# Kernel optimization log

Measured on AMD Instinct MI355X. Metric: run time of the kernel, lower is better.

## Reference

```python
import jax, jax.numpy as jnp
import numpy as np

K = 1254  # top-k patches kept by the gate


def setup_inputs() -> dict:
    key = jax.random.key(0)
    k1, k2 = jax.random.split(key)
    x = jax.random.normal(k1, (16, 224, 224, 64), dtype=jnp.float32)
    gating_kernel = jax.random.normal(k2, (2, 2, 64, 1), dtype=jnp.float32) * 0.05
    return {"x": x, "gating_kernel": gating_kernel}


def reference(x, gating_kernel):
    # x: [B, H, W, C] (NHWC), gating_kernel: [kh, kw, C, 1]
    B, H, W, C = x.shape
    kh, kw = gating_kernel.shape[0], gating_kernel.shape[1]
    # 1-channel gating conv, stride == kernel size, 'valid' padding -> [B, Ho, Wo]
    g = jax.lax.conv_general_dilated(
        x, gating_kernel,
        window_strides=(kh, kw), padding='VALID',
        dimension_numbers=('NHWC', 'HWIO', 'NHWC'))[..., 0]
    Ho, Wo = g.shape[1], g.shape[2]
    n = Ho * Wo
    flat = g.reshape(B, n)
    # top-k patch scores per image; activation is linear (None) in this config
    values, indices = jax.lax.top_k(flat, K)
    # scatter-sum values back to a dense [B, n] gate (top_k indices are distinct,
    # so add == unsorted_segment_sum exactly)
    batch_idx = jnp.arange(B)[:, None]  # [B, 1]
    gate = jnp.zeros((B, n), dtype=x.dtype).at[batch_idx, indices].add(values)
    gate = gate.reshape(B, Ho, Wo)
    # broadcast each patch score over its kh x kw spatial block and all C channels
    gate_full = jnp.broadcast_to(
        gate[:, :, None, :, None], (B, Ho, kh, Wo, kw)).reshape(B, H, W)
    return x * gate_full[..., None]
```

## Files before the change

kernel.cpp:

```cpp
#include <hip/hip_runtime.h>
#include <hip/hip_bf16.h>
#include <stdint.h>

#define BATCH   16
#define HDIM    224
#define WDIM    224
#define CDIM    64
#define HO      112
#define WO      112
#define NPATCH  (HO * WO)
#define KSEL    1254
#define ROWF    (WDIM * CDIM)
#define PERTHR  49
#define ROWF4   (WDIM * 16)
#define BLKROW  14

typedef float f32x4 __attribute__((ext_vector_type(4)));

__global__ __launch_bounds__(256) void conv_gate_kernel(
    const float* __restrict__ x, const float* __restrict__ wk,
    float* __restrict__ g) {
  const int tid = threadIdx.x;
  const int lane = tid & 31;
  const int p = blockIdx.x * 8 + (tid >> 5);

  const int b   = p / NPATCH;
  const int rem = p - b * NPATCH;
  const int ho  = rem / WO;
  const int wo  = rem - ho * WO;

  const float4 w0 = *reinterpret_cast<const float4*>(wk + lane * 4);
  const float4 w1 = *reinterpret_cast<const float4*>(wk + 128 + lane * 4);

  const long row0 = (long)(b * HDIM + 2 * ho) * ROWF + wo * 128 + lane * 4;
  const float4 a0 = *reinterpret_cast<const float4*>(x + row0);
  const float4 a1 = *reinterpret_cast<const float4*>(x + row0 + ROWF);

  float partial = a0.x * w0.x + a0.y * w0.y + a0.z * w0.z + a0.w * w0.w
                + a1.x * w1.x + a1.y * w1.y + a1.z * w1.z + a1.w * w1.w;

  #pragma unroll
  for (int off = 16; off > 0; off >>= 1)
    partial += __shfl_down(partial, off, 32);

  if (lane == 0) g[p] = partial;
}

__global__ __launch_bounds__(256) void select_kernel(
    const float* __restrict__ g, float* __restrict__ gate) {
  __shared__ int wave_cnt[4];
  __shared__ uint32_t sh_T;
  __shared__ int sh_cg;
  __shared__ int eq_list[256];
  __shared__ int eq_count;

  const int b = blockIdx.x;
  const int tid = threadIdx.x;
  const float* __restrict__ gb  = g    + b * NPATCH;
  float* __restrict__       gtb = gate + b * NPATCH;

  uint32_t key[PERTHR];
  #pragma unroll
  for (int j = 0; j < PERTHR; ++j) {
    uint32_t u = __float_as_uint(gb[tid + j * 256]);
    key[j] = (u & 0x80000000u) ? ~u : (u | 0x80000000u);
  }
  if (tid == 0) eq_count = 0;

  uint32_t T = 0;
  for (int bit = 31; bit >= 0; --bit) {
    const uint32_t cand = T | (1u << bit);
    int c = 0;
    #pragma unroll
    for (int j = 0; j < PERTHR; ++j) c += (key[j] >= cand) ? 1 : 0;
    #pragma unroll
    for (int off = 32; off > 0; off >>= 1) c += __shfl_down(c, off, 64);
    if ((tid & 63) == 0) wave_cnt[tid >> 6] = c;
    __syncthreads();
    if (tid == 0) {
      int tot = wave_cnt[0] + wave_cnt[1] + wave_cnt[2] + wave_cnt[3];
      sh_T = (tot >= KSEL) ? cand : T;
    }
    __syncthreads();
    T = sh_T;
  }

  {
    int c = 0;
    #pragma unroll
    for (int j = 0; j < PERTHR; ++j) c += (key[j] > T) ? 1 : 0;
    #pragma unroll
    for (int off = 32; off > 0; off >>= 1) c += __shfl_down(c, off, 64);
    if ((tid & 63) == 0) wave_cnt[tid >> 6] = c;
    __syncthreads();
    if (tid == 0) sh_cg = wave_cnt[0] + wave_cnt[1] + wave_cnt[2] + wave_cnt[3];
    __syncthreads();
  }
  const int krem = KSEL - sh_cg;

  #pragma unroll
  for (int j = 0; j < PERTHR; ++j) {
    const int i = tid + j * 256;
    const uint32_t k = key[j];
    float v = 0.0f;
    if (k > T) {
      uint32_t u = (k & 0x80000000u) ? (k & 0x7FFFFFFFu) : ~k;
      v = __uint_as_float(u);
    }
    gtb[i] = v;
    if (k == T) {
      int pos = atomicAdd(&eq_count, 1);
      if (pos < 256) eq_list[pos] = i;
    }
  }
  __syncthreads();

  if (tid == 0) {
    const int ec = eq_count;
    if (ec <= 256) {
      for (int i = 0; i < ec; ++i) {
        int mn = i;
        for (int j = i + 1; j < ec; ++j)
          if (eq_list[j] < eq_list[mn]) mn = j;
        int t = eq_list[mn]; eq_list[mn] = eq_list[i]; eq_list[i] = t;
      }
      for (int i = 0; i < ec && i < krem; ++i) {
        int idx = eq_list[i];
        uint32_t u = (T & 0x80000000u) ? (T & 0x7FFFFFFFu) : ~T;
        gtb[idx] = __uint_as_float(u);
      }
    } else {
      int kept = 0;
      for (int i = 0; i < NPATCH; ++i) {
        uint32_t u = __float_as_uint(gb[i]);
        uint32_t k = (u & 0x80000000u) ? ~u : (u | 0x80000000u);
        if (k == T) { gtb[i] = (kept < krem) ? gb[i] : 0.0f; ++kept; }
      }
    }
  }
}

__global__ __launch_bounds__(256) void apply_gate_kernel(
    const float* __restrict__ x, const float* __restrict__ gate,
    float* __restrict__ out) {
  const int bi = blockIdx.x;
  const int rowblk = bi % BLKROW;
  const int rowid  = bi / BLKROW;
  const int h = rowid % HDIM;
  const int b = rowid / HDIM;

  const int v4row = rowblk * 256 + threadIdx.x;
  const int w = v4row >> 4;
  const int gidx = b * NPATCH + (h >> 1) * WO + (w >> 1);

  const float gv = gate[gidx];
  const size_t v4 = (size_t)rowid * ROWF4 + v4row;

  f32x4 o = {0.0f, 0.0f, 0.0f, 0.0f};
  if (gv != 0.0f) {
    const f32x4 a = *reinterpret_cast<const f32x4*>(x + v4 * 4);
    o = a * gv;
  }
  __builtin_nontemporal_store(o, reinterpret_cast<f32x4*>(out + v4 * 4));
}

extern "C" void kernel_launch(void* const* d_in, const int* in_sizes, int n_in,
                              void* d_out, int out_size, void* d_ws, size_t ws_size,
                              hipStream_t stream) {
  const float* x  = (const float*)d_in[0];
  const float* wk = (const float*)d_in[1];
  float* out = (float*)d_out;

  float* g    = (float*)d_ws;
  float* gate = g + BATCH * NPATCH;

  conv_gate_kernel<<<(BATCH * NPATCH) / 8, 256, 0, stream>>>(x, wk, g);
  select_kernel<<<BATCH, 256, 0, stream>>>(g, gate);
  apply_gate_kernel<<<BATCH * HDIM * BLKROW, 256, 0, stream>>>(x, gate, out);
}
```

Measured before the change: 356.5 us.

## Shorten top-k radix select with 16-bit bucket and candidate refinement

```diff
diff --git a/kernel.cpp b/kernel.cpp
--- a/kernel.cpp
+++ b/kernel.cpp
@@ -11,9 +11,13 @@
 #define NPATCH  (HO * WO)
 #define KSEL    1254
 #define ROWF    (WDIM * CDIM)
-#define PERTHR  49
 #define ROWF4   (WDIM * 16)
 #define BLKROW  14
+
+#define STH     448
+#define SPT     28
+#define SWAVES  7
+#define CAP     1024
 
 typedef float f32x4 __attribute__((ext_vector_type(4)));
 
@@ -46,96 +50,150 @@
   if (lane == 0) g[p] = partial;
 }
 
-__global__ __launch_bounds__(256) void select_kernel(
+__global__ __launch_bounds__(STH) void select_kernel(
     const float* __restrict__ g, float* __restrict__ gate) {
-  __shared__ int wave_cnt[4];
+  __shared__ int cnt[2][SWAVES];
+  __shared__ int cand_cnt;
+  __shared__ uint32_t cand_key[CAP];
+  __shared__ int cand_idx[CAP];
+  __shared__ uint8_t used[CAP];
   __shared__ uint32_t sh_T;
-  __shared__ int sh_cg;
-  __shared__ int eq_list[256];
-  __shared__ int eq_count;
-
-  const int b = blockIdx.x;
-  const int tid = threadIdx.x;
+  __shared__ int sh_ntie;
+  __shared__ int sh_krem;
+  __shared__ int sh_over;
+
+  const int b = blockIdx.x, tid = threadIdx.x;
   const float* __restrict__ gb  = g    + b * NPATCH;
   float* __restrict__       gtb = gate + b * NPATCH;
 
-  uint32_t key[PERTHR];
-  #pragma unroll
-  for (int j = 0; j < PERTHR; ++j) {
-    uint32_t u = __float_as_uint(gb[tid + j * 256]);
+  uint32_t key[SPT];
+  #pragma unroll
+  for (int j = 0; j < SPT; ++j) {
+    uint32_t u = __float_as_uint(gb[tid + j * STH]);
     key[j] = (u & 0x80000000u) ? ~u : (u | 0x80000000u);
   }
-  if (tid == 0) eq_count = 0;
+  if (tid == 0) { cand_cnt = 0; sh_over = 0; }
 
   uint32_t T = 0;
-  for (int bit = 31; bit >= 0; --bit) {
-    const uint32_t cand = T | (1u << bit);
+  int par = 0;
+  auto block_count = [&](int c) -> int {
+    #pragma unroll
+    for (int off = 32; off > 0; off >>= 1) c += __shfl_down(c, off, 64);
+    if ((tid & 63) == 0) cnt[par][tid >> 6] = c;
+    __syncthreads();
+    int tot = 0;
+    #pragma unroll
+    for (int wv = 0; wv < SWAVES; ++wv) tot += cnt[par][wv];
+    par ^= 1;
+    return tot;
+  };
+
+  for (int bit = 31; bit >= 16; --bit) {
+    const uint32_t c0 = T | (1u << bit);
     int c = 0;
     #pragma unroll
-    for (int j = 0; j < PERTHR; ++j) c += (key[j] >= cand) ? 1 : 0;
-    #pragma unroll
-    for (int off = 32; off > 0; off >>= 1) c += __shfl_down(c, off, 64);
-    if ((tid & 63) == 0) wave_cnt[tid >> 6] = c;
+    for (int j = 0; j < SPT; ++j) c += (key[j] >= c0) ? 1 : 0;
+    if (block_count(c) >= KSEL) T = c0;
+  }
+
+  int c0n = 0;
+  {
+    const uint64_t U = (uint64_t)T + 0x10000ull;
+    #pragma unroll
+    for (int j = 0; j < SPT; ++j) c0n += ((uint64_t)key[j] >= U) ? 1 : 0;
+  }
+  const int cntU = block_count(c0n);
+  int krem = KSEL - cntU;
+
+  #pragma unroll
+  for (int j = 0; j < SPT; ++j) {
+    if ((key[j] & 0xFFFF0000u) == T) {
+      int pos = atomicAdd(&cand_cnt, 1);
+      if (pos < CAP) { cand_key[pos] = key[j]; cand_idx[pos] = tid + j * STH; }
+    }
+  }
+  __syncthreads();
+  int ncand = cand_cnt;
+
+  if (ncand > CAP) {
+    for (int bit = 15; bit >= 0; --bit) {
+      const uint32_t cc = T | (1u << bit);
+      int c = 0;
+      #pragma unroll
+      for (int j = 0; j < SPT; ++j) c += (key[j] >= cc) ? 1 : 0;
+      if (block_count(c) >= KSEL) T = cc;
+    }
+    int c2 = 0;
+    #pragma unroll
+    for (int j = 0; j < SPT; ++j) c2 += (key[j] > T) ? 1 : 0;
+    const int cg = block_count(c2);
+    krem = KSEL - cg;
+    if (tid == 0) cand_cnt = 0;
     __syncthreads();
-    if (tid == 0) {
-      int tot = wave_cnt[0] + wave_cnt[1] + wave_cnt[2] + wave_cnt[3];
-      sh_T = (tot >= KSEL) ? cand : T;
+    #pragma unroll
+    for (int j = 0; j < SPT; ++j) {
+      if (key[j] == T) {
+        int pos = atomicAdd(&cand_cnt, 1);
+        if (pos < CAP) { cand_key[pos] = key[j]; cand_idx[pos] = tid + j * STH; }
+      }
     }
     __syncthreads();
-    T = sh_T;
-  }
-
-  {
-    int c = 0;
-    #pragma unroll
-    for (int j = 0; j < PERTHR; ++j) c += (key[j] > T) ? 1 : 0;
-    #pragma unroll
-    for (int off = 32; off > 0; off >>= 1) c += __shfl_down(c, off, 64);
-    if ((tid & 63) == 0) wave_cnt[tid >> 6] = c;
-    __syncthreads();
-    if (tid == 0) sh_cg = wave_cnt[0] + wave_cnt[1] + wave_cnt[2] + wave_cnt[3];
-    __syncthreads();
-  }
-  const int krem = KSEL - sh_cg;
-
-  #pragma unroll
-  for (int j = 0; j < PERTHR; ++j) {
-    const int i = tid + j * 256;
+    ncand = cand_cnt;
+  }
+
+  if (tid == 0) {
+    if (ncand <= CAP) {
+      for (int i = 0; i < ncand; ++i) used[i] = 0;
+      uint32_t Tx = 0;
+      for (int t = 0; t < krem; ++t) {
+        int bi = -1; uint32_t bk = 0; int bidx = 0x7FFFFFFF;
+        for (int i = 0; i < ncand; ++i) {
+          if (used[i]) continue;
+          const uint32_t k = cand_key[i];
+          if (bi < 0 || k > bk || (k == bk && cand_idx[i] < bidx)) {
+            bi = i; bk = k; bidx = cand_idx[i];
+          }
+        }
+        used[bi] = 1; Tx = bk;
+      }
+      sh_T = Tx;
+      int nt = 0;
+      for (int i = 0; i < ncand; ++i)
+        if (used[i] && cand_key[i] == Tx) cand_idx[nt++] = cand_idx[i];
+      sh_ntie = nt;
+      sh_over = 0;
+    } else {
+      sh_T = T;
+      sh_over = 1;
+      sh_krem = krem;
+    }
+  }
+  __syncthreads();
+  const uint32_t Tf = sh_T;
+
+  #pragma unroll
+  for (int j = 0; j < SPT; ++j) {
+    const int i = tid + j * STH;
     const uint32_t k = key[j];
     float v = 0.0f;
-    if (k > T) {
+    if (k > Tf) {
       uint32_t u = (k & 0x80000000u) ? (k & 0x7FFFFFFFu) : ~k;
       v = __uint_as_float(u);
     }
     gtb[i] = v;
-    if (k == T) {
-      int pos = atomicAdd(&eq_count, 1);
-      if (pos < 256) eq_list[pos] = i;
-    }
   }
   __syncthreads();
 
-  if (tid == 0) {
-    const int ec = eq_count;
-    if (ec <= 256) {
-      for (int i = 0; i < ec; ++i) {
-        int mn = i;
-        for (int j = i + 1; j < ec; ++j)
-          if (eq_list[j] < eq_list[mn]) mn = j;
-        int t = eq_list[mn]; eq_list[mn] = eq_list[i]; eq_list[i] = t;
-      }
-      for (int i = 0; i < ec && i < krem; ++i) {
-        int idx = eq_list[i];
-        uint32_t u = (T & 0x80000000u) ? (T & 0x7FFFFFFFu) : ~T;
-        gtb[idx] = __uint_as_float(u);
-      }
-    } else {
-      int kept = 0;
-      for (int i = 0; i < NPATCH; ++i) {
-        uint32_t u = __float_as_uint(gb[i]);
-        uint32_t k = (u & 0x80000000u) ? ~u : (u | 0x80000000u);
-        if (k == T) { gtb[i] = (kept < krem) ? gb[i] : 0.0f; ++kept; }
-      }
+  const float tval =
+      __uint_as_float((Tf & 0x80000000u) ? (Tf & 0x7FFFFFFFu) : ~Tf);
+  if (!sh_over) {
+    for (int i = tid; i < sh_ntie; i += STH) gtb[cand_idx[i]] = tval;
+  } else if (tid == 0) {
+    int kept = 0; const int kr = sh_krem;
+    for (int i = 0; i < NPATCH && kept < kr; ++i) {
+      uint32_t u = __float_as_uint(gb[i]);
+      uint32_t k = (u & 0x80000000u) ? ~u : (u | 0x80000000u);
+      if (k == Tf) { gtb[i] = tval; ++kept; }
     }
   }
 }
@@ -175,6 +233,6 @@
   float* gate = g + BATCH * NPATCH;
 
   conv_gate_kernel<<<(BATCH * NPATCH) / 8, 256, 0, stream>>>(x, wk, g);
-  select_kernel<<<BATCH, 256, 0, stream>>>(g, gate);
+  select_kernel<<<BATCH, STH, 0, stream>>>(g, gate);
   apply_gate_kernel<<<BATCH * HDIM * BLKROW, 256, 0, stream>>>(x, gate, out);
 }
```

Measured after the change: 416.7 us. +16.9%, slower.
